# Kernel tuning notes

Measured on AMD Instinct MI355X. Metric: run time of the kernel, lower is better.

Reference implementation:

```python
import jax, jax.numpy as jnp
import numpy as np

S, B, H, NH, M = 2048, 2, 2048, 16, 2048
D = H // NH
FF = 4 * H
NORM = float(np.sqrt(D))  # norm_factor = sqrt(head_dim), no layer scaling
MASK_FILL = jnp.float32(-1e4)


def _ln(x, g, b):
    mu = jnp.mean(x, -1, keepdims=True)
    var = jnp.mean(jnp.square(x - mu), -1, keepdims=True)
    return (x - mu) * jax.lax.rsqrt(var + 1e-5) * g + b


def _l2(x):  # F.normalize over last dim
    return x * jax.lax.rsqrt(jnp.sum(jnp.square(x), -1, keepdims=True) + 1e-12)


def _mlp(h, w1, b1, w2, b2):  # ParallelMLP: h -> 4h -> h with gelu
    return jax.nn.gelu(h @ w1 + b1) @ w2 + b2


def setup_inputs() -> dict:
    key = jax.random.key(0)
    ks = jax.random.split(key, 12)
    w = lambda k, sh: jax.random.normal(k, sh, jnp.float32) * 0.02
    return {
        'x': jax.random.normal(ks[0], (S, B, H), jnp.float32),
        'mem_hidden': jax.random.normal(ks[1], (M, B, H), jnp.float32),
        'mem_mask': jax.random.randint(ks[2], (B, 1, S, M), 0, 5) == 0,  # True = masked
        'ln1_g': jnp.ones((H,), jnp.float32), 'ln1_b': jnp.zeros((H,), jnp.float32),
        'ln2_g': jnp.ones((H,), jnp.float32), 'ln2_b': jnp.zeros((H,), jnp.float32),
        'ln3_g': jnp.ones((H,), jnp.float32), 'ln3_b': jnp.zeros((H,), jnp.float32),
        'w_mlp1_in': w(ks[3], (H, FF)), 'b_mlp1_in': jnp.zeros((FF,), jnp.float32),
        'w_mlp1_out': w(ks[4], (FF, H)), 'b_mlp1_out': jnp.zeros((H,), jnp.float32),
        'w_q': w(ks[5], (H, H)), 'b_q': jnp.zeros((H,), jnp.float32),
        'w_kv': w(ks[6], (H, 2 * H)), 'b_kv': jnp.zeros((2 * H,), jnp.float32),
        'w_dense': w(ks[7], (H, H)), 'b_dense': jnp.zeros((H,), jnp.float32),
        'w_mlp2_in': w(ks[8], (H, FF)), 'b_mlp2_in': jnp.zeros((FF,), jnp.float32),
        'w_mlp2_out': w(ks[9], (FF, H)), 'b_mlp2_out': jnp.zeros((H,), jnp.float32),
    }


def reference(x, mem_hidden, mem_mask, ln1_g, ln1_b, ln2_g, ln2_b, ln3_g, ln3_b,
              w_mlp1_in, b_mlp1_in, w_mlp1_out, b_mlp1_out,
              w_q, b_q, w_kv, b_kv, w_dense, b_dense,
              w_mlp2_in, b_mlp2_in, w_mlp2_out, b_mlp2_out):
    # NOTE: source literally replaces x with mlp1 output (no residual on mlp1)
    x = _mlp(_ln(x, ln1_g, ln1_b), w_mlp1_in, b_mlp1_in, w_mlp1_out, b_mlp1_out)

    # memory attention: l2-normalized query vs l2-normalized retrieved memory k/v
    h2 = _ln(x, ln2_g, ln2_b)
    q = _l2((h2 @ w_q + b_q).reshape(S, B, NH, D))              # [s,b,h,d]
    kv = (mem_hidden @ w_kv + b_kv).reshape(M, B, NH, 2 * D)    # hidden_to_kv
    k = _l2(kv[..., :D])                                        # [m,b,h,d]
    v = _l2(kv[..., D:])
    scores = jnp.einsum('sbhd,mbhd->bhsm', q, k) / NORM
    scores = jnp.where(mem_mask, MASK_FILL, scores)             # attention_mask_func fill
    probs = jax.nn.softmax(scores, axis=-1)
    ctx = jnp.einsum('bhsm,mbhd->sbhd', probs, v).reshape(S, B, H)
    x = x + ctx @ w_dense + b_dense                             # dense w/ skip_bias_add

    x = x + _mlp(_ln(x, ln3_g, ln3_b), w_mlp2_in, b_mlp2_in, w_mlp2_out, b_mlp2_out)
    return x
```

## Files before the change

### kernel.cpp

```cpp
#include <hip/hip_runtime.h>
#include <stdint.h>
#include <stddef.h>

typedef __attribute__((ext_vector_type(8))) short bf16x8;
typedef __attribute__((ext_vector_type(4))) float f32x4;
typedef unsigned short u16;
typedef unsigned int u32;
typedef unsigned long long u64;

static constexpr int S_ = 2048, B_ = 2, H_ = 2048, NH_ = 16, D_ = 128, M_ = 2048, FF_ = 8192;
static constexpr int SB_ = S_ * B_;
static constexpr int MB_ = M_ * B_;

__device__ __forceinline__ float b2f(u16 b) {
  union { u32 u; float f; } v; v.u = ((u32)b) << 16; return v.f;
}
__device__ __forceinline__ u16 f2b(float f) {
  union { float f; u32 u; } v; v.f = f;
  u32 u = v.u;
  return (u16)((u + 0x7FFFu + ((u >> 16) & 1u)) >> 16);
}
__device__ __forceinline__ float geluf(float x) {
  float x3 = x * x * x;
  return 0.5f * x * (1.0f + tanhf(0.7978845608028654f * (x + 0.044715f * x3)));
}

#define LDSP(p) (reinterpret_cast<__attribute__((address_space(3))) uint32_t*>(reinterpret_cast<uintptr_t>(p)))
#define GLBP(p) (reinterpret_cast<const __attribute__((address_space(1))) uint32_t*>(reinterpret_cast<uintptr_t>(p)))

__global__ void detect_kinds(const u32* __restrict__ x0, const u32* __restrict__ mask, int* __restrict__ flags) {
  if (threadIdx.x == 0 && blockIdx.x == 0) {
    int cnt = 0;
    for (int i = 0; i < 256; ++i) {
      u32 e = (x0[i] >> 7) & 0xFFu;
      if (e >= 118u && e <= 130u) ++cnt;
    }
    flags[0] = (cnt >= 128) ? 0 : 1;
    int all01 = 1, allf = 1, allb = 1;
    for (int i = 0; i < 256; ++i) {
      u32 v = mask[i];
      if (v > 1u) all01 = 0;
      if (v != 0u && v != 0x3F800000u) allf = 0;
      u32 lo = v & 0xFFFFu, hi = v >> 16;
      if ((lo != 0u && lo != 0x3F80u) || (hi != 0u && hi != 0x3F80u)) allb = 0;
    }
    flags[1] = all01 ? 1 : (allf ? 3 : (allb ? 2 : 0));
  }
}

__global__ void mask_bits(const void* __restrict__ mraw, const int* __restrict__ flags, u64* __restrict__ bm) {
  int i = blockIdx.x * 256 + threadIdx.x;
  int kind = flags[1];
  int masked;
  if (kind == 1)      masked = ((const int*)mraw)[i] != 0;
  else if (kind == 3) masked = ((const float*)mraw)[i] != 0.0f;
  else if (kind == 2) masked = ((const u16*)mraw)[i] != 0;
  else                masked = ((const unsigned char*)mraw)[i] != 0;
  u64 vote = __ballot(masked == 0);
  if ((threadIdx.x & 63) == 0) bm[i >> 6] = vote;
}

__global__ void cvt_all(const void* s0, const void* s1, const void* s2, const void* s3,
                        const void* s4, const void* s5, const void* s6, const void* s7,
                        const void* s8, const void* s9, const void* s10, const void* s11,
                        const void* s12, const int* __restrict__ flags, float* __restrict__ SM) {
  const int i = blockIdx.x * 256 + threadIdx.x;
  if (i >= 40960) return;
  const void* src; int off;
  if (i < 8192)       { src = s0;  off = 0; }
  else if (i < 10240) { src = s1;  off = 8192; }
  else if (i < 12288) { src = s2;  off = 10240; }
  else if (i < 16384) { src = s3;  off = 12288; }
  else if (i < 18432) { src = s4;  off = 16384; }
  else if (i < 26624) { src = s5;  off = 18432; }
  else if (i < 28672) { src = s6;  off = 26624; }
  else if (i < 30720) { src = s7;  off = 28672; }
  else if (i < 32768) { src = s8;  off = 30720; }
  else if (i < 34816) { src = s9;  off = 32768; }
  else if (i < 36864) { src = s10; off = 34816; }
  else if (i < 38912) { src = s11; off = 36864; }
  else                { src = s12; off = 38912; }
  const int j = i - off;
  SM[i] = flags[0] ? ((const float*)src)[j] : b2f(((const u16*)src)[j]);
}

__global__ void cast_in_bf16(const void* __restrict__ src, const int* __restrict__ flags, u16* __restrict__ dst, int n8) {
  int i = blockIdx.x * 256 + threadIdx.x;
  if (i >= n8) return;
  if (flags[0]) {
    const float4* p = (const float4*)src;
    float4 a = p[i * 2], c = p[i * 2 + 1];
    bf16x8 o;
    o[0] = (short)f2b(a.x); o[1] = (short)f2b(a.y); o[2] = (short)f2b(a.z); o[3] = (short)f2b(a.w);
    o[4] = (short)f2b(c.x); o[5] = (short)f2b(c.y); o[6] = (short)f2b(c.z); o[7] = (short)f2b(c.w);
    *(bf16x8*)&dst[i * 8] = o;
  } else {
    *(bf16x8*)&dst[i * 8] = ((const bf16x8*)src)[i];
  }
}

__global__ __launch_bounds__(256) void transpose_cast(const void* __restrict__ in, const int* __restrict__ flags,
                                                      u16* __restrict__ out, int R, int C) {
  __shared__ u16 tile[64][65];
  const int isf = flags[0];
  const int tr = blockIdx.y * 64, tc = blockIdx.x * 64;
  const int tx = threadIdx.x & 63, ty = threadIdx.x >> 6;
  const float* inf = (const float*)in;
  const u16* inb = (const u16*)in;
#pragma unroll
  for (int i = 0; i < 16; ++i) {
    int r = ty * 16 + i;
    size_t idx = (size_t)(tr + r) * C + tc + tx;
    tile[r][tx] = isf ? f2b(inf[idx]) : inb[idx];
  }
  __syncthreads();
#pragma unroll
  for (int i = 0; i < 16; ++i) {
    int c = ty * 16 + i;
    out[(size_t)(tc + c) * R + tr + tx] = tile[tx][c];
  }
}

template <int EXT>
__global__ __launch_bounds__(256) void layernorm_k(const void* __restrict__ xin, const int* __restrict__ flags,
                                                   const float* __restrict__ g, const float* __restrict__ bta,
                                                   u16* __restrict__ out) {
  const int row = blockIdx.x, t = threadIdx.x;
  float v[8];
  bool bfmode = EXT && (flags[0] == 0);
  if (bfmode) {
    const u16* xr = (const u16*)xin + (size_t)row * H_ + t * 8;
    bf16x8 a = *(const bf16x8*)xr;
#pragma unroll
    for (int j = 0; j < 8; ++j) v[j] = b2f((u16)a[j]);
  } else {
    const float* xr = (const float*)xin + (size_t)row * H_ + t * 8;
    float4 a = *(const float4*)xr, c = *(const float4*)(xr + 4);
    v[0] = a.x; v[1] = a.y; v[2] = a.z; v[3] = a.w;
    v[4] = c.x; v[5] = c.y; v[6] = c.z; v[7] = c.w;
  }
  float s1 = 0.f, s2 = 0.f;
#pragma unroll
  for (int j = 0; j < 8; ++j) { s1 += v[j]; s2 += v[j] * v[j]; }
#pragma unroll
  for (int off = 32; off > 0; off >>= 1) { s1 += __shfl_down(s1, off); s2 += __shfl_down(s2, off); }
  __shared__ float red[8];
  const int w = t >> 6;
  if ((t & 63) == 0) { red[w] = s1; red[4 + w] = s2; }
  __syncthreads();
  s1 = red[0] + red[1] + red[2] + red[3];
  s2 = red[4] + red[5] + red[6] + red[7];
  const float mean = s1 * (1.0f / H_);
  const float rstd = rsqrtf(s2 * (1.0f / H_) - mean * mean + 1e-5f);
  bf16x8 o;
#pragma unroll
  for (int j = 0; j < 8; ++j) {
    float y = (v[j] - mean) * rstd * g[t * 8 + j] + bta[t * 8 + j];
    o[j] = (short)f2b(y);
  }
  *(bf16x8*)(out + (size_t)row * H_ + t * 8) = o;
}

template <int BN, int GELU, int RES, int WF, int WB, int ODYN>
__global__ __launch_bounds__(512, 2) void gemm8p(const u16* __restrict__ A, const u16* __restrict__ Bt,
                                                 const float* __restrict__ bias, const float* __restrict__ res,
                                                 void* __restrict__ outF, u16* __restrict__ outB,
                                                 const int* __restrict__ flags, int Mr, int N, int K) {
  constexpr int NBF = (BN == 256) ? 2 : 1;
  __shared__ u16 lds[65536];
  const int t = threadIdx.x;
  const int w = t >> 6, l = t & 63, lr = l & 15, lk = l >> 4;
  const int wr = w >> 2, wc = w & 3;
  const int gx = gridDim.x, gy = gridDim.y;
  const int orig = blockIdx.y * gx + blockIdx.x;
  const int nwg = gx * gy, per = nwg >> 3;
  int tm, tn;
  {
    const int xcd = orig & 7, p = orig >> 3;
    const int ncx = gx >> 3 ? gx >> 3 : 1;
    if ((gx & 7) == 0 && (per & 7) == 0) {
      const int cy = per >> 3;
      const int ccol = xcd % ncx, crow = xcd / ncx;
      const int px = p & 7, py = p >> 3;
      tn = (ccol * 8 + px) * BN;
      tm = (crow * cy + py) * 256;
    } else {
      tn = (orig % gx) * BN;
      tm = (orig / gx) * 256;
    }
  }
  const int r0 = t >> 3;
  const int cl = (t & 7) ^ (r0 & 7);
  const u32 abase = (u32)(tm + r0) * (u32)K + (u32)cl * 8;
  const u32 bbase = (u32)(tn + r0) * (u32)K + (u32)cl * 8;
  const int wdst = w * 512;
  const int cso0 = ((0 + lk) ^ (lr & 7)) * 8;
  const int cso1 = ((4 + lk) ^ (lr & 7)) * 8;
  const int brow0 = (BN == 256) ? ((wc & 1) * 64) : (wc * 32);

  const int NT = K >> 6, NI = NT >> 1;
  f32x4 acc[8][2 * NBF] = {};

#define STGA_(h) do { if ((h) < 2 * NT) {                                                              \
    const int sl_ = ((h) & 3) * 8192;                                                                  \
    const u32 so_ = abase + ((u32)((h) & 1) * 128u) * (u32)K + ((u32)((h) >> 1)) * 64u;                \
    __builtin_amdgcn_global_load_lds(GLBP(A + so_), LDSP(lds + sl_ + wdst), 16, 0, 0);                 \
    __builtin_amdgcn_global_load_lds(GLBP(A + so_ + (u32)64 * (u32)K), LDSP(lds + sl_ + 4096 + wdst), 16, 0, 0); \
  } } while (0)
#define STGB_(h) do {                                                                                  \
    if constexpr (BN == 256) { if ((h) < 2 * NT) {                                                     \
      const int sl_ = 32768 + ((h) & 3) * 8192;                                                        \
      const u32 so_ = bbase + ((u32)((h) & 1) * 128u) * (u32)K + ((u32)((h) >> 1)) * 64u;              \
      __builtin_amdgcn_global_load_lds(GLBP(Bt + so_), LDSP(lds + sl_ + wdst), 16, 0, 0);              \
      __builtin_amdgcn_global_load_lds(GLBP(Bt + so_ + (u32)64 * (u32)K), LDSP(lds + sl_ + 4096 + wdst), 16, 0, 0); \
    } } else { if ((h) < NT) {                                                                         \
      const int sl_ = 32768 + ((h) & 3) * 8192;                                                        \
      const u32 so_ = bbase + ((u32)(h)) * 64u;                                                        \
      __builtin_amdgcn_global_load_lds(GLBP(Bt + so_), LDSP(lds + sl_ + wdst), 16, 0, 0);              \
      __builtin_amdgcn_global_load_lds(GLBP(Bt + so_ + (u32)64 * (u32)K), LDSP(lds + sl_ + 4096 + wdst), 16, 0, 0); \
    } }                                                                                                \
  } while (0)
#define RDA_(dst, mh, sa)                                                                              \
  _Pragma("unroll") for (int mf2 = 0; mf2 < 4; ++mf2) {                                                \
    const u16* p_ = lds + (sa) * 8192 + ((mh) * 64 + mf2 * 16 + lr) * 64;                              \
    dst[mf2][0] = *(const bf16x8*)(p_ + cso0);                                                         \
    dst[mf2][1] = *(const bf16x8*)(p_ + cso1); }
#define RDB_(dst, nh, sb)                                                                              \
  _Pragma("unroll") for (int nf2 = 0; nf2 < NBF; ++nf2) {                                              \
    const u16* p_ = lds + 32768 + (sb) * 8192 + (brow0 + ((nh) * NBF + nf2) * 16 + lr) * 64;           \
    dst[nf2][0] = *(const bf16x8*)(p_ + cso0);                                                         \
    dst[nf2][1] = *(const bf16x8*)(p_ + cso1); }
#define MM_(afX, bqX, mh, nh)                                                                          \
  _Pragma("unroll") for (int kk = 0; kk < 2; ++kk)                                                     \
  _Pragma("unroll") for (int mf2 = 0; mf2 < 4; ++mf2)                                                  \
  _Pragma("unroll") for (int nf2 = 0; nf2 < NBF; ++nf2)                                                \
    acc[(mh) * 4 + mf2][(nh) * NBF + nf2] = __builtin_amdgcn_mfma_f32_16x16x32_bf16(                   \
        afX[mf2][kk], bqX[nf2][kk], acc[(mh) * 4 + mf2][(nh) * NBF + nf2], 0, 0, 0);
#define PHASE_MID()                                                                                    \
  __builtin_amdgcn_s_barrier();                                                                        \
  asm volatile("s_waitcnt lgkmcnt(0)" ::: "memory");                                                   \
  __builtin_amdgcn_sched_barrier(0);                                                                   \
  __builtin_amdgcn_s_setprio(1);
#define PHASE_END()                                                                                    \
  __builtin_amdgcn_s_setprio(0);                                                                       \
  __builtin_amdgcn_s_barrier();
#define VMW_FULL()                                                                                     \
  if constexpr (BN == 256) { asm volatile("s_waitcnt vmcnt(8)" ::: "memory"); }                        \
  else                     { asm volatile("s_waitcnt vmcnt(6)" ::: "memory"); }

  if constexpr (BN == 256) {
    STGB_(0); STGB_(1); STGA_(0); STGA_(1);
    STGB_(2); STGB_(3); STGA_(2); STGA_(3);
    asm volatile("s_waitcnt vmcnt(8)" ::: "memory");
  } else {
    STGB_(0); STGA_(0); STGA_(1);
    STGB_(1); STGA_(2); STGA_(3);
    asm volatile("s_waitcnt vmcnt(6)" ::: "memory");
  }
  __builtin_amdgcn_s_barrier();

  for (int it = 0; it < NI; ++it) {
    const int T0 = it * 2;
    bf16x8 af[4][2], bq0[NBF][2], bq1[NBF][2];

    {
      const int sa = (2 * T0 + wr) & 3;
      const int sb = (BN == 256) ? ((2 * T0 + (wc >> 1)) & 3) : (T0 & 3);
      RDA_(af, 0, sa); RDB_(bq0, 0, sb);
      PHASE_MID(); MM_(af, bq0, 0, 0); PHASE_END();
      RDB_(bq1, 1, sb);
      PHASE_MID(); MM_(af, bq1, 0, 1); PHASE_END();
      RDA_(af, 1, sa);
      if constexpr (BN == 256) { STGB_(2 * T0 + 4); STGB_(2 * T0 + 5); }
      else                     { STGB_(T0 + 2); }
      PHASE_MID(); MM_(af, bq0, 1, 0); PHASE_END();
      STGA_(2 * T0 + 4); STGA_(2 * T0 + 5);
      __builtin_amdgcn_s_barrier();
      __builtin_amdgcn_s_setprio(1);
      MM_(af, bq1, 1, 1);
      __builtin_amdgcn_s_setprio(0);
      if (T0 + 2 < NT) { VMW_FULL(); }
      else             { asm volatile("s_waitcnt vmcnt(0)" ::: "memory"); }
      __builtin_amdgcn_s_barrier();
    }
    {
      const int T1 = T0 + 1;
      const int sa = (2 * T1 + wr) & 3;
      const int sb = (BN == 256) ? ((2 * T1 + (wc >> 1)) & 3) : (T1 & 3);
      RDA_(af, 0, sa); RDB_(bq0, 0, sb);
      PHASE_MID(); MM_(af, bq0, 0, 0); PHASE_END();
      RDB_(bq1, 1, sb);
      PHASE_MID(); MM_(af, bq1, 0, 1); PHASE_END();
      RDA_(af, 1, sa);
      if constexpr (BN == 256) { STGB_(2 * T1 + 4); STGB_(2 * T1 + 5); }
      else                     { STGB_(T1 + 2); }
      PHASE_MID(); MM_(af, bq0, 1, 0); PHASE_END();
      STGA_(2 * T1 + 4); STGA_(2 * T1 + 5);
      __builtin_amdgcn_s_barrier();
      __builtin_amdgcn_s_setprio(1);
      MM_(af, bq1, 1, 1);
      __builtin_amdgcn_s_setprio(0);
      if (T1 + 2 < NT) { VMW_FULL(); }
      else             { asm volatile("s_waitcnt vmcnt(0)" ::: "memory"); }
      __builtin_amdgcn_s_barrier();
    }
  }
#undef STGA_
#undef STGB_
#undef RDA_
#undef RDB_
#undef MM_
#undef PHASE_MID
#undef PHASE_END
#undef VMW_FULL

  const int obf = ODYN ? (flags[0] ? 0 : 1) : 0;
  (void)Mr;
#pragma unroll
  for (int mf = 0; mf < 8; ++mf) {
#pragma unroll
    for (int nf = 0; nf < 2 * NBF; ++nf) {
      const int col = tn + wc * (BN == 256 ? 64 : 32) + nf * 16 + lr;
      const float bv = bias[col];
#pragma unroll
      for (int j = 0; j < 4; ++j) {
        const int rw = tm + wr * 128 + mf * 16 + lk * 4 + j;
        float vv = acc[mf][nf][j] + bv;
        if (RES) vv += res[(size_t)rw * N + col];
        if (GELU) vv = geluf(vv);
        if (WF) {
          if (ODYN && obf) ((u16*)outF)[(size_t)rw * N + col] = f2b(vv);
          else ((float*)outF)[(size_t)rw * N + col] = vv;
        }
        if (WB) outB[(size_t)rw * N + col] = f2b(vv);
      }
    }
  }
}

__global__ __launch_bounds__(256) void l2_q(const float* __restrict__ qpre, u16* __restrict__ Q) {
  const int t = threadIdx.x;
  const int g = blockIdx.x * 64 + (t >> 2);
  const int lg = t & 3;
  const int h = g & (NH_ - 1), sb = g >> 4;
  const float* p = qpre + (size_t)sb * H_ + h * D_ + lg * 32;
  float vv[32];
  float ss = 0.f;
#pragma unroll
  for (int i = 0; i < 8; ++i) {
    float4 a = *(const float4*)&p[i * 4];
    vv[i * 4 + 0] = a.x; vv[i * 4 + 1] = a.y; vv[i * 4 + 2] = a.z; vv[i * 4 + 3] = a.w;
    ss += a.x * a.x + a.y * a.y + a.z * a.z + a.w * a.w;
  }
  ss += __shfl_xor(ss, 1); ss += __shfl_xor(ss, 2);
  const float sc = rsqrtf(ss + 1e-12f);
  const int s = sb >> 1, b = sb & 1;
  u16* o = Q + ((size_t)(b * NH_ + h) * S_ + s) * D_ + lg * 32;
#pragma unroll
  for (int i = 0; i < 4; ++i) {
    bf16x8 ov;
#pragma unroll
    for (int j = 0; j < 8; ++j) ov[j] = (short)f2b(vv[i * 8 + j] * sc);
    *(bf16x8*)&o[i * 8] = ov;
  }
}

__global__ __launch_bounds__(256) void l2_kv(const float* __restrict__ kvpre, u16* __restrict__ Kq, u16* __restrict__ Vt) {
  __shared__ u16 vtT[128][72];
  const int t = threadIdx.x;
  const int bid = blockIdx.x;
  const int mt = bid & 31, h = (bid >> 5) & 15, b = bid >> 9;
  const int lm = t >> 2, lg = t & 3;
  const int m = mt * 64 + lm;
  const size_t rowoff = (size_t)(m * B_ + b) * (2 * H_) + h * 256;
  float vv[32];
  {
    const float* p = kvpre + rowoff + lg * 32;
    float ss = 0.f;
#pragma unroll
    for (int i = 0; i < 8; ++i) {
      float4 a = *(const float4*)&p[i * 4];
      vv[i * 4 + 0] = a.x; vv[i * 4 + 1] = a.y; vv[i * 4 + 2] = a.z; vv[i * 4 + 3] = a.w;
      ss += a.x * a.x + a.y * a.y + a.z * a.z + a.w * a.w;
    }
    ss += __shfl_xor(ss, 1); ss += __shfl_xor(ss, 2);
    const float sc = rsqrtf(ss + 1e-12f);
    u16* o = Kq + ((size_t)(b * NH_ + h) * M_ + m) * D_ + lg * 32;
#pragma unroll
    for (int i = 0; i < 4; ++i) {
      bf16x8 ov;
#pragma unroll
      for (int j = 0; j < 8; ++j) ov[j] = (short)f2b(vv[i * 8 + j] * sc);
      *(bf16x8*)&o[i * 8] = ov;
    }
  }
  {
    const float* p = kvpre + rowoff + 128 + lg * 32;
    float ss = 0.f;
#pragma unroll
    for (int i = 0; i < 8; ++i) {
      float4 a = *(const float4*)&p[i * 4];
      vv[i * 4 + 0] = a.x; vv[i * 4 + 1] = a.y; vv[i * 4 + 2] = a.z; vv[i * 4 + 3] = a.w;
      ss += a.x * a.x + a.y * a.y + a.z * a.z + a.w * a.w;
    }
    ss += __shfl_xor(ss, 1); ss += __shfl_xor(ss, 2);
    const float sc = rsqrtf(ss + 1e-12f);
#pragma unroll
    for (int i = 0; i < 32; ++i) vtT[lg * 32 + i][lm] = f2b(vv[i] * sc);
  }
  __syncthreads();
  const int d = t >> 1, half = t & 1;
  u16* o = Vt + ((size_t)(b * NH_ + h) * D_ + d) * M_ + mt * 64 + half * 32;
#pragma unroll
  for (int i = 0; i < 4; ++i) {
    bf16x8 ov = *(const bf16x8*)&vtT[d][half * 32 + i * 8];
    *(bf16x8*)&o[i * 8] = ov;
  }
}

__global__ __launch_bounds__(256, 3) void attn_k(const u16* __restrict__ Q, const u16* __restrict__ Kq,
                                                 const u16* __restrict__ Vt, const u32* __restrict__ BM32,
                                                 u16* __restrict__ ctx) {
  __shared__ u16 Kl[2][4096];
  __shared__ u16 Vl[2][4096];
  __shared__ u16 Pl[4][16 * 40];
  const int t = threadIdx.x, w = t >> 6, l = t & 63, lr = l & 15, lk = l >> 4;
  const int lin = blockIdx.x;
  const int xcd = lin & 7, idx = lin >> 3;
  const int bh = xcd * 4 + (idx >> 5);
  const int chunk = idx & 31;
  const int b = bh >> 4, h = bh & 15;
  const int srow = chunk * 64 + w * 16;
  const u16* Qb = Q + ((size_t)bh * S_ + srow) * D_;
  bf16x8 qf[4];
#pragma unroll
  for (int kc = 0; kc < 4; ++kc)
    qf[kc] = *(const bf16x8*)&Qb[lr * D_ + kc * 32 + lk * 8];
  f32x4 oacc[8] = {};
  float den[4] = {};
  const u16* Kb = Kq + (size_t)bh * M_ * D_;
  const u16* Vb = Vt + (size_t)bh * D_ * M_;
  const float invn = 0.08838834764831845f;
  u32 ksrc[2], vsrc[2];
#pragma unroll
  for (int i = 0; i < 2; ++i) {
    const int kidx = i * 256 + t;
    const int kr = kidx >> 4, kc_ = (kidx & 15) ^ (kr & 7);
    ksrc[i] = (u32)kr * D_ + (u32)kc_ * 8;
    const int vidx = i * 256 + t;
    const int vd = vidx >> 2, vc = (vidx & 3) ^ ((vd >> 1) & 3);
    vsrc[i] = (u32)vd * M_ + (u32)vc * 8;
  }
  const int wdst = w * 64 * 8;
  u32 mrow[4];
#pragma unroll
  for (int j2 = 0; j2 < 4; ++j2)
    mrow[j2] = ((u32)b * S_ + (u32)(srow + lk * 4 + j2)) * 64u;

#define STG(buf, m0) do {                                                                              \
    _Pragma("unroll")                                                                                  \
    for (int i = 0; i < 2; ++i) {                                                                      \
      __builtin_amdgcn_global_load_lds(GLBP(Kb + (size_t)(m0) * D_ + ksrc[i]),                         \
                                       LDSP(&Kl[buf][i * 2048 + wdst]), 16, 0, 0);                     \
      __builtin_amdgcn_global_load_lds(GLBP(Vb + (size_t)(m0) + vsrc[i]),                              \
                                       LDSP(&Vl[buf][i * 2048 + wdst]), 16, 0, 0);                     \
    }                                                                                                  \
  } while (0)

  STG(0, 0);
  asm volatile("s_waitcnt vmcnt(0)" ::: "memory");
  __builtin_amdgcn_s_barrier();
  int cur = 0;

  for (int t64 = 0; t64 < M_ / 32; ++t64) {
    const int m0 = t64 * 32;
    if (t64 + 1 < M_ / 32) STG(cur ^ 1, m0 + 32);
    u32 mw[4];
#pragma unroll
    for (int j2 = 0; j2 < 4; ++j2) mw[j2] = BM32[mrow[j2] + t64];
    f32x4 sc[2] = {};
#pragma unroll
    for (int mf = 0; mf < 2; ++mf) {
      const int r = mf * 16 + lr;
#pragma unroll
      for (int kc = 0; kc < 4; ++kc) {
        const int cc = ((kc * 4 + lk) ^ (r & 7));
        bf16x8 kfv = *(const bf16x8*)&Kl[cur][r * 128 + cc * 8];
        sc[mf] = __builtin_amdgcn_mfma_f32_16x16x32_bf16(qf[kc], kfv, sc[mf], 0, 0, 0);
      }
    }
#pragma unroll
    for (int j2 = 0; j2 < 4; ++j2) {
      const int rloc = lk * 4 + j2;
#pragma unroll
      for (int mf = 0; mf < 2; ++mf) {
        float p = __expf(sc[mf][j2] * invn);
        p = ((mw[j2] >> (mf * 16 + lr)) & 1u) ? p : 0.0f;
        den[j2] += p;
        Pl[w][rloc * 40 + mf * 16 + lr] = f2b(p);
      }
    }
    asm volatile("s_waitcnt lgkmcnt(0)" ::: "memory");
    __builtin_amdgcn_sched_barrier(0);
    bf16x8 pa = *(const bf16x8*)&Pl[w][lr * 40 + lk * 8];
#pragma unroll
    for (int nf = 0; nf < 8; ++nf) {
      const int d = nf * 16 + lr;
      const int cc = lk ^ ((d >> 1) & 3);
      bf16x8 vfv = *(const bf16x8*)&Vl[cur][d * 32 + cc * 8];
      oacc[nf] = __builtin_amdgcn_mfma_f32_16x16x32_bf16(pa, vfv, oacc[nf], 0, 0, 0);
    }
    asm volatile("s_waitcnt vmcnt(0)" ::: "memory");
    __builtin_amdgcn_s_barrier();
    cur ^= 1;
  }
#undef STG
#pragma unroll
  for (int j2 = 0; j2 < 4; ++j2) {
    float d = den[j2];
    d += __shfl_xor(d, 1); d += __shfl_xor(d, 2); d += __shfl_xor(d, 4); d += __shfl_xor(d, 8);
    den[j2] = 1.0f / fmaxf(d, 1e-20f);
  }
#pragma unroll
  for (int nf = 0; nf < 8; ++nf)
#pragma unroll
    for (int j2 = 0; j2 < 4; ++j2) {
      const int s = srow + lk * 4 + j2;
      const int dd = nf * 16 + lr;
      ctx[((size_t)s * B_ + b) * H_ + h * D_ + dd] = f2b(oacc[nf][j2] * den[j2]);
    }
}

extern "C" void kernel_launch(void* const* d_in, const int* in_sizes, int n_in,
                              void* d_out, int out_size, void* d_ws, size_t ws_size,
                              hipStream_t stream) {
  (void)in_sizes; (void)n_in; (void)out_size; (void)ws_size;
  char* ws = (char*)d_ws;
  u16* WT     = (u16*)(ws + 0);
  void* MID   = (void*)(ws + 33554432);
  float* XF   = (float*)(ws + 100663296);
  u16* HB     = (u16*)(ws + 134217728);
  u16* MEMB   = (u16*)(ws + 150994944);
  u16* QB     = (u16*)(ws + 167772160);
  u16* KB     = (u16*)(ws + 184549376);
  u16* VTB    = (u16*)(ws + 201326592);
  u64* BMB    = (u64*)(ws + 218103808);
  float* SM   = (float*)(ws + 234881024);
  int* FLAGS  = (int*)(ws + 235044864);

  float* Bias1  = SM + 0;
  float* Bias1o = SM + 8192;
  float* BiasQ  = SM + 10240;
  float* BiasKV = SM + 12288;
  float* BiasD  = SM + 16384;
  float* Bias2  = SM + 18432;
  float* Bias2o = SM + 26624;
  float* G1v = SM + 28672; float* B1v = SM + 30720;
  float* G2v = SM + 32768; float* B2v = SM + 34816;
  float* G3v = SM + 36864; float* B3v = SM + 38912;

  detect_kinds<<<1, 64, 0, stream>>>((const u32*)d_in[0], (const u32*)d_in[2], FLAGS);

  cvt_all<<<160, 256, 0, stream>>>(d_in[10], d_in[12], d_in[14], d_in[16], d_in[18],
                                   d_in[20], d_in[22], d_in[3], d_in[4], d_in[5],
                                   d_in[6], d_in[7], d_in[8], FLAGS, SM);

  mask_bits<<<(B_ * S_ * M_) / 256, 256, 0, stream>>>(d_in[2], FLAGS, BMB);
  cast_in_bf16<<<(MB_ * H_ / 8) / 256, 256, 0, stream>>>(d_in[1], FLAGS, MEMB, MB_ * H_ / 8);

  dim3 blk(256);
  dim3 blk5(512);
  layernorm_k<1><<<SB_, blk, 0, stream>>>(d_in[0], FLAGS, G1v, B1v, HB);
  transpose_cast<<<dim3(FF_ / 64, H_ / 64), blk, 0, stream>>>(d_in[9], FLAGS, WT, H_, FF_);
  gemm8p<256, 1, 0, 0, 1, 0><<<dim3(FF_ / 256, SB_ / 256), blk5, 0, stream>>>(HB, WT, Bias1, nullptr, nullptr, (u16*)MID, FLAGS, SB_, FF_, H_);
  transpose_cast<<<dim3(H_ / 64, FF_ / 64), blk, 0, stream>>>(d_in[11], FLAGS, WT, FF_, H_);
  gemm8p<128, 0, 0, 1, 0, 0><<<dim3(H_ / 128, SB_ / 256), blk5, 0, stream>>>((u16*)MID, WT, Bias1o, nullptr, XF, nullptr, FLAGS, SB_, H_, FF_);

  layernorm_k<0><<<SB_, blk, 0, stream>>>(XF, FLAGS, G2v, B2v, HB);
  transpose_cast<<<dim3(H_ / 64, H_ / 64), blk, 0, stream>>>(d_in[13], FLAGS, WT, H_, H_);
  gemm8p<128, 0, 0, 1, 0, 0><<<dim3(H_ / 128, SB_ / 256), blk5, 0, stream>>>(HB, WT, BiasQ, nullptr, MID, nullptr, FLAGS, SB_, H_, H_);
  l2_q<<<(SB_ * NH_) / 64, blk, 0, stream>>>((const float*)MID, QB);
  transpose_cast<<<dim3(2 * H_ / 64, H_ / 64), blk, 0, stream>>>(d_in[15], FLAGS, WT, H_, 2 * H_);
  gemm8p<256, 0, 0, 1, 0, 0><<<dim3(2 * H_ / 256, MB_ / 256), blk5, 0, stream>>>(MEMB, WT, BiasKV, nullptr, MID, nullptr, FLAGS, MB_, 2 * H_, H_);
  l2_kv<<<B_ * NH_ * (M_ / 64), blk, 0, stream>>>((const float*)MID, KB, VTB);
  attn_k<<<1024, blk, 0, stream>>>(QB, KB, VTB, (const u32*)BMB, MEMB);
  transpose_cast<<<dim3(H_ / 64, H_ / 64), blk, 0, stream>>>(d_in[17], FLAGS, WT, H_, H_);
  gemm8p<128, 0, 1, 1, 0, 0><<<dim3(H_ / 128, SB_ / 256), blk5, 0, stream>>>(MEMB, WT, BiasD, XF, XF, nullptr, FLAGS, SB_, H_, H_);

  layernorm_k<0><<<SB_, blk, 0, stream>>>(XF, FLAGS, G3v, B3v, HB);
  transpose_cast<<<dim3(FF_ / 64, H_ / 64), blk, 0, stream>>>(d_in[19], FLAGS, WT, H_, FF_);
  gemm8p<256, 1, 0, 0, 1, 0><<<dim3(FF_ / 256, SB_ / 256), blk5, 0, stream>>>(HB, WT, Bias2, nullptr, nullptr, (u16*)MID, FLAGS, SB_, FF_, H_);
  transpose_cast<<<dim3(H_ / 64, FF_ / 64), blk, 0, stream>>>(d_in[21], FLAGS, WT, FF_, H_);
  gemm8p<128, 0, 1, 1, 0, 1><<<dim3(H_ / 128, SB_ / 256), blk5, 0, stream>>>((u16*)MID, WT, Bias2o, XF, d_out, nullptr, FLAGS, SB_, H_, FF_);
}
```

Baseline: 1.251 ms.

## Replace 8-wave 256-tile GEMM with simpler 4-wave 128x128 double-buffered GEMM

Swaps the 512-thread gemm8p kernel (256xBN tiles, 4-stage LDS ring, phased barrier schedule) for a 256-thread 128x128-tile kernel with two LDS buffers and register double-buffering of fragments across the two K halves. It uses half the LDS per block and launches four times as many smaller blocks, which may raise occupancy and improve load balance across CUs. In exchange it gives up data reuse per tile and the deeper prefetch, and it waits for all outstanding global loads each K step, which can leave memory latency exposed.

Result: faster. 1.152 ms (-7.9%).

```diff
diff --git a/kernel.cpp b/kernel.cpp
--- a/kernel.cpp
+++ b/kernel.cpp
@@ -161,170 +161,119 @@
   *(bf16x8*)(out + (size_t)row * H_ + t * 8) = o;
 }
 
-template <int BN, int GELU, int RES, int WF, int WB, int ODYN>
-__global__ __launch_bounds__(512, 2) void gemm8p(const u16* __restrict__ A, const u16* __restrict__ Bt,
+template <int GELU, int RES, int WF, int WB, int ODYN>
+__global__ __launch_bounds__(256, 2) void gemmra(const u16* __restrict__ A, const u16* __restrict__ Bt,
                                                  const float* __restrict__ bias, const float* __restrict__ res,
                                                  void* __restrict__ outF, u16* __restrict__ outB,
                                                  const int* __restrict__ flags, int Mr, int N, int K) {
-  constexpr int NBF = (BN == 256) ? 2 : 1;
-  __shared__ u16 lds[65536];
+  __shared__ u16 lds[32768];
   const int t = threadIdx.x;
   const int w = t >> 6, l = t & 63, lr = l & 15, lk = l >> 4;
-  const int wr = w >> 2, wc = w & 3;
+  const int wr = w >> 1, wc = w & 1;
   const int gx = gridDim.x, gy = gridDim.y;
   const int orig = blockIdx.y * gx + blockIdx.x;
   const int nwg = gx * gy, per = nwg >> 3;
   int tm, tn;
-  {
+  if ((gx & 7) == 0 && (per & 7) == 0) {
     const int xcd = orig & 7, p = orig >> 3;
-    const int ncx = gx >> 3 ? gx >> 3 : 1;
-    if ((gx & 7) == 0 && (per & 7) == 0) {
-      const int cy = per >> 3;
-      const int ccol = xcd % ncx, crow = xcd / ncx;
-      const int px = p & 7, py = p >> 3;
-      tn = (ccol * 8 + px) * BN;
-      tm = (crow * cy + py) * 256;
-    } else {
-      tn = (orig % gx) * BN;
-      tm = (orig / gx) * 256;
-    }
-  }
-  const int r0 = t >> 3;
-  const int cl = (t & 7) ^ (r0 & 7);
-  const u32 abase = (u32)(tm + r0) * (u32)K + (u32)cl * 8;
-  const u32 bbase = (u32)(tn + r0) * (u32)K + (u32)cl * 8;
+    const int ncx = gx >> 3, cy = per >> 3;
+    const int ccol = xcd % ncx, crow = xcd / ncx;
+    const int px = p & 7, py = p >> 3;
+    tn = (ccol * 8 + px) * 128;
+    tm = (crow * cy + py) * 128;
+  } else {
+    tn = (orig % gx) * 128;
+    tm = (orig / gx) * 128;
+  }
+  u32 aofs[4], bofs[4];
+#pragma unroll
+  for (int i = 0; i < 4; ++i) {
+    const int idx = i * 256 + t;
+    const int srow = idx >> 3, sc = idx & 7;
+    const int lc = sc ^ (srow & 7);
+    aofs[i] = (u32)(tm + srow) * (u32)K + (u32)lc * 8;
+    bofs[i] = (u32)(tn + srow) * (u32)K + (u32)lc * 8;
+  }
   const int wdst = w * 512;
   const int cso0 = ((0 + lk) ^ (lr & 7)) * 8;
   const int cso1 = ((4 + lk) ^ (lr & 7)) * 8;
-  const int brow0 = (BN == 256) ? ((wc & 1) * 64) : (wc * 32);
-
-  const int NT = K >> 6, NI = NT >> 1;
-  f32x4 acc[8][2 * NBF] = {};
-
-#define STGA_(h) do { if ((h) < 2 * NT) {                                                              \
-    const int sl_ = ((h) & 3) * 8192;                                                                  \
-    const u32 so_ = abase + ((u32)((h) & 1) * 128u) * (u32)K + ((u32)((h) >> 1)) * 64u;                \
-    __builtin_amdgcn_global_load_lds(GLBP(A + so_), LDSP(lds + sl_ + wdst), 16, 0, 0);                 \
-    __builtin_amdgcn_global_load_lds(GLBP(A + so_ + (u32)64 * (u32)K), LDSP(lds + sl_ + 4096 + wdst), 16, 0, 0); \
-  } } while (0)
-#define STGB_(h) do {                                                                                  \
-    if constexpr (BN == 256) { if ((h) < 2 * NT) {                                                     \
-      const int sl_ = 32768 + ((h) & 3) * 8192;                                                        \
-      const u32 so_ = bbase + ((u32)((h) & 1) * 128u) * (u32)K + ((u32)((h) >> 1)) * 64u;              \
-      __builtin_amdgcn_global_load_lds(GLBP(Bt + so_), LDSP(lds + sl_ + wdst), 16, 0, 0);              \
-      __builtin_amdgcn_global_load_lds(GLBP(Bt + so_ + (u32)64 * (u32)K), LDSP(lds + sl_ + 4096 + wdst), 16, 0, 0); \
-    } } else { if ((h) < NT) {                                                                         \
-      const int sl_ = 32768 + ((h) & 3) * 8192;                                                        \
-      const u32 so_ = bbase + ((u32)(h)) * 64u;                                                        \
-      __builtin_amdgcn_global_load_lds(GLBP(Bt + so_), LDSP(lds + sl_ + wdst), 16, 0, 0);              \
-      __builtin_amdgcn_global_load_lds(GLBP(Bt + so_ + (u32)64 * (u32)K), LDSP(lds + sl_ + 4096 + wdst), 16, 0, 0); \
-    } }                                                                                                \
+  int arow[4], brow[4];
+#pragma unroll
+  for (int f = 0; f < 4; ++f) {
+    arow[f] = (wr * 64 + f * 16 + lr) * 64;
+    brow[f] = (wc * 64 + f * 16 + lr) * 64;
+  }
+
+  const int NS = K >> 6;
+  f32x4 acc[4][4] = {};
+
+#define STG(sl) do {                                                                                  \
+    u16* Ad = lds + ((sl) & 1) * 16384;                                                               \
+    u16* Bd = Ad + 8192;                                                                              \
+    const u32 ko = (u32)(sl) * 64;                                                                    \
+    _Pragma("unroll")                                                                                 \
+    for (int i = 0; i < 4; ++i) {                                                                     \
+      __builtin_amdgcn_global_load_lds(GLBP(A + aofs[i] + ko), LDSP(Ad + i * 2048 + wdst), 16, 0, 0); \
+      __builtin_amdgcn_global_load_lds(GLBP(Bt + bofs[i] + ko), LDSP(Bd + i * 2048 + wdst), 16, 0, 0);\
+    }                                                                                                 \
   } while (0)
-#define RDA_(dst, mh, sa)                                                                              \
-  _Pragma("unroll") for (int mf2 = 0; mf2 < 4; ++mf2) {                                                \
-    const u16* p_ = lds + (sa) * 8192 + ((mh) * 64 + mf2 * 16 + lr) * 64;                              \
-    dst[mf2][0] = *(const bf16x8*)(p_ + cso0);                                                         \
-    dst[mf2][1] = *(const bf16x8*)(p_ + cso1); }
-#define RDB_(dst, nh, sb)                                                                              \
-  _Pragma("unroll") for (int nf2 = 0; nf2 < NBF; ++nf2) {                                              \
-    const u16* p_ = lds + 32768 + (sb) * 8192 + (brow0 + ((nh) * NBF + nf2) * 16 + lr) * 64;           \
-    dst[nf2][0] = *(const bf16x8*)(p_ + cso0);                                                         \
-    dst[nf2][1] = *(const bf16x8*)(p_ + cso1); }
-#define MM_(afX, bqX, mh, nh)                                                                          \
-  _Pragma("unroll") for (int kk = 0; kk < 2; ++kk)                                                     \
-  _Pragma("unroll") for (int mf2 = 0; mf2 < 4; ++mf2)                                                  \
-  _Pragma("unroll") for (int nf2 = 0; nf2 < NBF; ++nf2)                                                \
-    acc[(mh) * 4 + mf2][(nh) * NBF + nf2] = __builtin_amdgcn_mfma_f32_16x16x32_bf16(                   \
-        afX[mf2][kk], bqX[nf2][kk], acc[(mh) * 4 + mf2][(nh) * NBF + nf2], 0, 0, 0);
-#define PHASE_MID()                                                                                    \
-  __builtin_amdgcn_s_barrier();                                                                        \
-  asm volatile("s_waitcnt lgkmcnt(0)" ::: "memory");                                                   \
-  __builtin_amdgcn_sched_barrier(0);                                                                   \
-  __builtin_amdgcn_s_setprio(1);
-#define PHASE_END()                                                                                    \
-  __builtin_amdgcn_s_setprio(0);                                                                       \
+#define RD(afX, bqX, sl, cso) do {                                                                    \
+    const u16* As_ = lds + ((sl) & 1) * 16384;                                                        \
+    const u16* Bs_ = As_ + 8192;                                                                      \
+    _Pragma("unroll")                                                                                 \
+    for (int f = 0; f < 4; ++f) {                                                                     \
+      afX[f] = *(const bf16x8*)(As_ + arow[f] + (cso));                                               \
+      bqX[f] = *(const bf16x8*)(Bs_ + brow[f] + (cso));                                               \
+    }                                                                                                 \
+  } while (0)
+#define MM(afX, bqX)                                                                                  \
+  _Pragma("unroll") for (int nf = 0; nf < 4; ++nf)                                                    \
+  _Pragma("unroll") for (int mf = 0; mf < 4; ++mf)                                                    \
+    acc[mf][nf] = __builtin_amdgcn_mfma_f32_16x16x32_bf16(afX[mf], bqX[nf], acc[mf][nf], 0, 0, 0);
+
+  bf16x8 afA[4], bqA[4], afB[4], bqB[4];
+
+  STG(0);
+  asm volatile("s_waitcnt vmcnt(0)" ::: "memory");
   __builtin_amdgcn_s_barrier();
-#define VMW_FULL()                                                                                     \
-  if constexpr (BN == 256) { asm volatile("s_waitcnt vmcnt(8)" ::: "memory"); }                        \
-  else                     { asm volatile("s_waitcnt vmcnt(6)" ::: "memory"); }
-
-  if constexpr (BN == 256) {
-    STGB_(0); STGB_(1); STGA_(0); STGA_(1);
-    STGB_(2); STGB_(3); STGA_(2); STGA_(3);
-    asm volatile("s_waitcnt vmcnt(8)" ::: "memory");
-  } else {
-    STGB_(0); STGA_(0); STGA_(1);
-    STGB_(1); STGA_(2); STGA_(3);
-    asm volatile("s_waitcnt vmcnt(6)" ::: "memory");
-  }
-  __builtin_amdgcn_s_barrier();
-
-  for (int it = 0; it < NI; ++it) {
-    const int T0 = it * 2;
-    bf16x8 af[4][2], bq0[NBF][2], bq1[NBF][2];
-
-    {
-      const int sa = (2 * T0 + wr) & 3;
-      const int sb = (BN == 256) ? ((2 * T0 + (wc >> 1)) & 3) : (T0 & 3);
-      RDA_(af, 0, sa); RDB_(bq0, 0, sb);
-      PHASE_MID(); MM_(af, bq0, 0, 0); PHASE_END();
-      RDB_(bq1, 1, sb);
-      PHASE_MID(); MM_(af, bq1, 0, 1); PHASE_END();
-      RDA_(af, 1, sa);
-      if constexpr (BN == 256) { STGB_(2 * T0 + 4); STGB_(2 * T0 + 5); }
-      else                     { STGB_(T0 + 2); }
-      PHASE_MID(); MM_(af, bq0, 1, 0); PHASE_END();
-      STGA_(2 * T0 + 4); STGA_(2 * T0 + 5);
-      __builtin_amdgcn_s_barrier();
-      __builtin_amdgcn_s_setprio(1);
-      MM_(af, bq1, 1, 1);
-      __builtin_amdgcn_s_setprio(0);
-      if (T0 + 2 < NT) { VMW_FULL(); }
-      else             { asm volatile("s_waitcnt vmcnt(0)" ::: "memory"); }
-      __builtin_amdgcn_s_barrier();
-    }
-    {
-      const int T1 = T0 + 1;
-      const int sa = (2 * T1 + wr) & 3;
-      const int sb = (BN == 256) ? ((2 * T1 + (wc >> 1)) & 3) : (T1 & 3);
-      RDA_(af, 0, sa); RDB_(bq0, 0, sb);
-      PHASE_MID(); MM_(af, bq0, 0, 0); PHASE_END();
-      RDB_(bq1, 1, sb);
-      PHASE_MID(); MM_(af, bq1, 0, 1); PHASE_END();
-      RDA_(af, 1, sa);
-      if constexpr (BN == 256) { STGB_(2 * T1 + 4); STGB_(2 * T1 + 5); }
-      else                     { STGB_(T1 + 2); }
-      PHASE_MID(); MM_(af, bq0, 1, 0); PHASE_END();
-      STGA_(2 * T1 + 4); STGA_(2 * T1 + 5);
-      __builtin_amdgcn_s_barrier();
-      __builtin_amdgcn_s_setprio(1);
-      MM_(af, bq1, 1, 1);
-      __builtin_amdgcn_s_setprio(0);
-      if (T1 + 2 < NT) { VMW_FULL(); }
-      else             { asm volatile("s_waitcnt vmcnt(0)" ::: "memory"); }
-      __builtin_amdgcn_s_barrier();
-    }
-  }
-#undef STGA_
-#undef STGB_
-#undef RDA_
-#undef RDB_
-#undef MM_
-#undef PHASE_MID
-#undef PHASE_END
-#undef VMW_FULL
+  RD(afA, bqA, 0, cso0);
+  asm volatile("s_waitcnt lgkmcnt(0)" ::: "memory");
+  __builtin_amdgcn_sched_barrier(0);
+
+  for (int s = 0; s < NS; ++s) {
+    if (s + 1 < NS) STG(s + 1);
+    RD(afB, bqB, s, cso1);
+    __builtin_amdgcn_sched_barrier(0);
+    __builtin_amdgcn_s_setprio(1);
+    MM(afA, bqA);
+    __builtin_amdgcn_s_setprio(0);
+    asm volatile("s_waitcnt lgkmcnt(0)" ::: "memory");
+    __builtin_amdgcn_sched_barrier(0);
+    asm volatile("s_waitcnt vmcnt(0)" ::: "memory");
+    __builtin_amdgcn_s_barrier();
+    if (s + 1 < NS) RD(afA, bqA, s + 1, cso0);
+    __builtin_amdgcn_sched_barrier(0);
+    __builtin_amdgcn_s_setprio(1);
+    MM(afB, bqB);
+    __builtin_amdgcn_s_setprio(0);
+    asm volatile("s_waitcnt lgkmcnt(0)" ::: "memory");
+    __builtin_amdgcn_sched_barrier(0);
+  }
+#undef STG
+#undef RD
+#undef MM
 
   const int obf = ODYN ? (flags[0] ? 0 : 1) : 0;
   (void)Mr;
 #pragma unroll
-  for (int mf = 0; mf < 8; ++mf) {
-#pragma unroll
-    for (int nf = 0; nf < 2 * NBF; ++nf) {
-      const int col = tn + wc * (BN == 256 ? 64 : 32) + nf * 16 + lr;
+  for (int mf = 0; mf < 4; ++mf) {
+#pragma unroll
+    for (int nf = 0; nf < 4; ++nf) {
+      const int col = tn + wc * 64 + nf * 16 + lr;
       const float bv = bias[col];
 #pragma unroll
       for (int j = 0; j < 4; ++j) {
-        const int rw = tm + wr * 128 + mf * 16 + lk * 4 + j;
+        const int rw = tm + wr * 64 + mf * 16 + lk * 4 + j;
         float vv = acc[mf][nf][j] + bv;
         if (RES) vv += res[(size_t)rw * N + col];
         if (GELU) vv = geluf(vv);
@@ -569,27 +518,26 @@
   cast_in_bf16<<<(MB_ * H_ / 8) / 256, 256, 0, stream>>>(d_in[1], FLAGS, MEMB, MB_ * H_ / 8);
 
   dim3 blk(256);
-  dim3 blk5(512);
   layernorm_k<1><<<SB_, blk, 0, stream>>>(d_in[0], FLAGS, G1v, B1v, HB);
   transpose_cast<<<dim3(FF_ / 64, H_ / 64), blk, 0, stream>>>(d_in[9], FLAGS, WT, H_, FF_);
-  gemm8p<256, 1, 0, 0, 1, 0><<<dim3(FF_ / 256, SB_ / 256), blk5, 0, stream>>>(HB, WT, Bias1, nullptr, nullptr, (u16*)MID, FLAGS, SB_, FF_, H_);
+  gemmra<1, 0, 0, 1, 0><<<dim3(FF_ / 128, SB_ / 128), blk, 0, stream>>>(HB, WT, Bias1, nullptr, nullptr, (u16*)MID, FLAGS, SB_, FF_, H_);
   transpose_cast<<<dim3(H_ / 64, FF_ / 64), blk, 0, stream>>>(d_in[11], FLAGS, WT, FF_, H_);
-  gemm8p<128, 0, 0, 1, 0, 0><<<dim3(H_ / 128, SB_ / 256), blk5, 0, stream>>>((u16*)MID, WT, Bias1o, nullptr, XF, nullptr, FLAGS, SB_, H_, FF_);
+  gemmra<0, 0, 1, 0, 0><<<dim3(H_ / 128, SB_ / 128), blk, 0, stream>>>((u16*)MID, WT, Bias1o, nullptr, XF, nullptr, FLAGS, SB_, H_, FF_);
 
   layernorm_k<0><<<SB_, blk, 0, stream>>>(XF, FLAGS, G2v, B2v, HB);
   transpose_cast<<<dim3(H_ / 64, H_ / 64), blk, 0, stream>>>(d_in[13], FLAGS, WT, H_, H_);
-  gemm8p<128, 0, 0, 1, 0, 0><<<dim3(H_ / 128, SB_ / 256), blk5, 0, stream>>>(HB, WT, BiasQ, nullptr, MID, nullptr, FLAGS, SB_, H_, H_);
+  gemmra<0, 0, 1, 0, 0><<<dim3(H_ / 128, SB_ / 128), blk, 0, stream>>>(HB, WT, BiasQ, nullptr, MID, nullptr, FLAGS, SB_, H_, H_);
   l2_q<<<(SB_ * NH_) / 64, blk, 0, stream>>>((const float*)MID, QB);
   transpose_cast<<<dim3(2 * H_ / 64, H_ / 64), blk, 0, stream>>>(d_in[15], FLAGS, WT, H_, 2 * H_);
-  gemm8p<256, 0, 0, 1, 0, 0><<<dim3(2 * H_ / 256, MB_ / 256), blk5, 0, stream>>>(MEMB, WT, BiasKV, nullptr, MID, nullptr, FLAGS, MB_, 2 * H_, H_);
+  gemmra<0, 0, 1, 0, 0><<<dim3(2 * H_ / 128, MB_ / 128), blk, 0, stream>>>(MEMB, WT, BiasKV, nullptr, MID, nullptr, FLAGS, MB_, 2 * H_, H_);
   l2_kv<<<B_ * NH_ * (M_ / 64), blk, 0, stream>>>((const float*)MID, KB, VTB);
   attn_k<<<1024, blk, 0, stream>>>(QB, KB, VTB, (const u32*)BMB, MEMB);
   transpose_cast<<<dim3(H_ / 64, H_ / 64), blk, 0, stream>>>(d_in[17], FLAGS, WT, H_, H_);
-  gemm8p<128, 0, 1, 1, 0, 0><<<dim3(H_ / 128, SB_ / 256), blk5, 0, stream>>>(MEMB, WT, BiasD, XF, XF, nullptr, FLAGS, SB_, H_, H_);
+  gemmra<0, 1, 1, 0, 0><<<dim3(H_ / 128, SB_ / 128), blk, 0, stream>>>(MEMB, WT, BiasD, XF, XF, nullptr, FLAGS, SB_, H_, H_);
 
   layernorm_k<0><<<SB_, blk, 0, stream>>>(XF, FLAGS, G3v, B3v, HB);
   transpose_cast<<<dim3(FF_ / 64, H_ / 64), blk, 0, stream>>>(d_in[19], FLAGS, WT, H_, FF_);
-  gemm8p<256, 1, 0, 0, 1, 0><<<dim3(FF_ / 256, SB_ / 256), blk5, 0, stream>>>(HB, WT, Bias2, nullptr, nullptr, (u16*)MID, FLAGS, SB_, FF_, H_);
+  gemmra<1, 0, 0, 1, 0><<<dim3(FF_ / 128, SB_ / 128), blk, 0, stream>>>(HB, WT, Bias2, nullptr, nullptr, (u16*)MID, FLAGS, SB_, FF_, H_);
   transpose_cast<<<dim3(H_ / 64, FF_ / 64), blk, 0, stream>>>(d_in[21], FLAGS, WT, FF_, H_);
-  gemm8p<128, 0, 1, 1, 0, 1><<<dim3(H_ / 128, SB_ / 256), blk5, 0, stream>>>((u16*)MID, WT, Bias2o, XF, d_out, nullptr, FLAGS, SB_, H_, FF_);
-}
+  gemmra<0, 1, 1, 0, 1><<<dim3(H_ / 128, SB_ / 128), blk, 0, stream>>>((u16*)MID, WT, Bias2o, XF, d_out, nullptr, FLAGS, SB_, H_, FF_);
+}
```
